# Optimization experiments

Measured on AMD Instinct MI355X. Metric: run time of the kernel, lower is better.

## Reference

```python
import jax, jax.numpy as jnp
import numpy as np

IN_F, OUT_F = 4096, 11008
IN_G, OUT_G = 8, 1
NUM_CB, CB_SIZE = 2, 256


def setup_inputs() -> dict:
    key = jax.random.key(0)
    k1, k2, k3, k4, k5 = jax.random.split(key, 5)
    no, ni = OUT_F // OUT_G, IN_F // IN_G
    x = jax.random.normal(k1, (4, 2048, IN_F), dtype=jnp.float32)
    codes = jax.random.randint(k2, (no, ni, NUM_CB), 0, CB_SIZE, dtype=jnp.int32)
    codebooks = jax.random.normal(k3, (NUM_CB, CB_SIZE, OUT_G, IN_G), dtype=jnp.float32)
    scales = jax.random.uniform(k4, (no, 1, 1, 1), dtype=jnp.float32) + 0.5
    bias = jax.random.normal(k5, (OUT_F,), dtype=jnp.float32)
    return {"x": x, "codes": codes, "codebooks": codebooks, "scales": scales, "bias": bias}


def _dequantize_weight(codes, codebooks, scales):
    # codes: [no, ni, M] ints; codebooks: [M, C, og, ig]; scales: [no, 1, 1, 1]
    M = codebooks.shape[0]
    og, ig = codebooks.shape[2], codebooks.shape[3]
    no, ni = codes.shape[0], codes.shape[1]
    # gather each codebook's entry and sum over codebooks -> [no, ni, og, ig]
    m_idx = jnp.arange(M)[None, None, :]
    gathered = codebooks[m_idx, codes]            # [no, ni, M, og, ig]
    deq = gathered.sum(axis=2) * scales           # [no, ni, og, ig]
    # reorder groups back to dense weight [out_features, in_features]
    return deq.transpose(0, 2, 1, 3).reshape(no * og, ni * ig)


def reference(x, codes, codebooks, scales, bias):
    w = _dequantize_weight(codes, codebooks, scales)  # [OUT_F, IN_F]
    return jnp.einsum("bsi,oi->bso", x, w) + bias
```

## Files before the change

### kernel.cpp

```cpp
#include <hip/hip_runtime.h>
#include <hip/hip_bf16.h>
#include <stdint.h>

#define IN_F   4096
#define OUT_F  11008
#define M_TOK  8192

typedef __attribute__((ext_vector_type(4))) int   int32x4;

__device__ __forceinline__ float block_rowmax(float m, float* red, int t) {
    red[t] = m; __syncthreads();
    for (int s = 128; s > 0; s >>= 1) {
        if (t < s) red[t] = fmaxf(red[t], red[t + s]);
        __syncthreads();
    }
    float r = red[0]; __syncthreads();
    return fmaxf(r, 1e-8f);
}

__global__ __launch_bounds__(256) void k_qx(
        const float* __restrict__ x, signed char* __restrict__ Xq,
        float* __restrict__ sx) {
    __shared__ float red[256];
    int r = blockIdx.x, t = threadIdx.x;
    const float4* xr = (const float4*)(x + (size_t)r * IN_F) + t * 4;
    float4 v0 = xr[0], v1 = xr[1], v2 = xr[2], v3 = xr[3];
    float m = 0.f;
#define MX4(v) m = fmaxf(m, fmaxf(fmaxf(fabsf(v.x), fabsf(v.y)), fmaxf(fabsf(v.z), fabsf(v.w))))
    MX4(v0); MX4(v1); MX4(v2); MX4(v3);
    float rm = block_rowmax(m, red, t);
    if (t == 0) sx[r] = rm / 127.f;
    float inv = 127.f / rm;
    union { signed char c[16]; uint4 u; } pk;
#define Q4(v, o) pk.c[o] = (signed char)__float2int_rn(v.x * inv);            \
                 pk.c[o+1] = (signed char)__float2int_rn(v.y * inv);          \
                 pk.c[o+2] = (signed char)__float2int_rn(v.z * inv);          \
                 pk.c[o+3] = (signed char)__float2int_rn(v.w * inv)
    Q4(v0, 0); Q4(v1, 4); Q4(v2, 8); Q4(v3, 12);
    *(uint4*)(Xq + (size_t)r * IN_F + t * 16) = pk.u;
}

__global__ __launch_bounds__(256) void k_qw(
        const int* __restrict__ codes,
        const float* __restrict__ codebooks,
        const float* __restrict__ scales,
        signed char* __restrict__ Wq, float* __restrict__ sw) {
    __shared__ float cb[4096];
    __shared__ float red[256];
    int o = blockIdx.x, t = threadIdx.x;
    {
        const float4* cbg = (const float4*)codebooks;
        float4* cbl = (float4*)cb;
#pragma unroll
        for (int i = 0; i < 4; ++i) cbl[t + i * 256] = cbg[t + i * 256];
    }
    __syncthreads();
    const int2* cp = (const int2*)codes + (size_t)o * 512 + t * 2;
    int2 c0 = cp[0], c1 = cp[1];
    float e[16]; float m = 0.f;
#pragma unroll
    for (int j = 0; j < 8; ++j) {
        e[j]     = cb[c0.x * 8 + j] + cb[2048 + c0.y * 8 + j];
        e[8 + j] = cb[c1.x * 8 + j] + cb[2048 + c1.y * 8 + j];
    }
#pragma unroll
    for (int j = 0; j < 16; ++j) m = fmaxf(m, fabsf(e[j]));
    float rm = block_rowmax(m, red, t);
    if (t == 0) sw[o] = scales[o] * rm / 127.f;
    float inv = 127.f / rm;
    union { signed char c[16]; uint4 u; } pk;
#pragma unroll
    for (int j = 0; j < 16; ++j) pk.c[j] = (signed char)__float2int_rn(e[j] * inv);
    *(uint4*)(Wq + (size_t)o * IN_F + t * 16) = pk.u;
}


#define BARRIER() __builtin_amdgcn_s_barrier()
#define VMW(n)    asm volatile("s_waitcnt vmcnt(" #n ")")

#define GL16(gp, lp) __builtin_amdgcn_global_load_lds(                        \
    (const __attribute__((address_space(1))) void*)(gp),                      \
    (__attribute__((address_space(3))) void*)(lp), 16, 0, 0)

__global__ __launch_bounds__(512, 2) void k_gemm(
        const signed char* __restrict__ A,
        const signed char* __restrict__ B,
        const float* __restrict__ sx,
        const float* __restrict__ sw,
        const float* __restrict__ bias,
        float* __restrict__ out) {
    __shared__ signed char lA0[256 * 128];
    __shared__ signed char lA1[256 * 128];
    __shared__ signed char lB0[256 * 128];
    __shared__ signed char lB1[256 * 128];

    const int tid = threadIdx.x;
    const int l = tid & 63;
    const int w = tid >> 6;
    const int wm = w >> 2, wn = w & 3;

    int lid = blockIdx.x;
    int xcd = lid & 7, j = lid >> 3;
    int bx = j >> 2;
    int by = (xcd << 2) + (j & 3);
    const int rowBase = by * 256;
    const int colBase = bx * 256;

    const int srow = w * 8 + (l >> 3);
    const int scol = ((l & 7) ^ ((l >> 3) & 7)) << 4;
    const signed char* gA = A + (size_t)(rowBase + srow) * IN_F + scol;
    const signed char* gB = B + (size_t)(colBase + srow) * IN_F + scol;
    signed char* lA0w = &lA0[w * 8 * 128];
    signed char* lA1w = &lA1[w * 8 * 128];
    signed char* lB0w = &lB0[w * 8 * 128];
    signed char* lB1w = &lB1[w * 8 * 128];

#define STAGEQ_(P, t, q) do {                                                 \
    const signed char* _g = (((q) < 2) ? gA : gB) + (size_t)(t) * 128;        \
    signed char* _l = (((q) < 2) ? lA##P##w : lB##P##w);                      \
    const int _r = ((q) & 1) * 128;                                           \
    GL16(_g + (size_t)_r * IN_F,        _l + _r * 128);                       \
    GL16(_g + (size_t)(_r + 64) * IN_F, _l + (_r + 64) * 128);                \
} while (0)

    const int frow = l & 15, g = l >> 4;
    const int cho0 = ((g ^ (frow & 7)) << 4);
    const int cho1 = (((4 + g) ^ (frow & 7)) << 4);
    const char* rowA0 = (const char*)&lA0[(wm * 128 + frow) * 128];
    const char* rowA1 = (const char*)&lA1[(wm * 128 + frow) * 128];
    const char* rowB0 = (const char*)&lB0[(wn * 64 + frow) * 128];
    const char* rowB1 = (const char*)&lB1[(wn * 64 + frow) * 128];
#define LDA_(P, m, kk) (*(const int32x4*)(rowA##P + (m) * 2048 + ((kk) ? cho1 : cho0)))
#define LDB_(P, n, kk) (*(const int32x4*)(rowB##P + (n) * 2048 + ((kk) ? cho1 : cho0)))

    int32x4 acc[8][4] = {};
    int32x4 ar[4][2], br[4][2];

#define QUAD(M0, N0) do {                                                     \
    __builtin_amdgcn_s_setprio(1);                                            \
    _Pragma("unroll") for (int mm = 0; mm < 4; ++mm)                          \
    _Pragma("unroll") for (int nn = 0; nn < 2; ++nn)                          \
    _Pragma("unroll") for (int kk = 0; kk < 2; ++kk)                          \
        acc[(M0) + mm][(N0) + nn] = __builtin_amdgcn_mfma_i32_16x16x64_i8(    \
            ar[mm][kk], br[(N0) + nn][kk], acc[(M0) + mm][(N0) + nn], 0, 0, 0);\
    __builtin_amdgcn_s_setprio(0);                                            \
} while (0)

#define RD_A03_B01(P) do {                                                    \
    _Pragma("unroll") for (int mm = 0; mm < 4; ++mm) {                        \
        ar[mm][0] = LDA_(P, mm, 0); ar[mm][1] = LDA_(P, mm, 1); }             \
    br[0][0] = LDB_(P, 0, 0); br[0][1] = LDB_(P, 0, 1);                       \
    br[1][0] = LDB_(P, 1, 0); br[1][1] = LDB_(P, 1, 1);                       \
} while (0)
#define RD_B23(P) do {                                                        \
    br[2][0] = LDB_(P, 2, 0); br[2][1] = LDB_(P, 2, 1);                       \
    br[3][0] = LDB_(P, 3, 0); br[3][1] = LDB_(P, 3, 1);                       \
} while (0)
#define RD_A47(P) do {                                                        \
    _Pragma("unroll") for (int mm = 0; mm < 4; ++mm) {                        \
        ar[mm][0] = LDA_(P, 4 + mm, 0); ar[mm][1] = LDA_(P, 4 + mm, 1); }     \
} while (0)

    STAGEQ_(0, 0, 0); STAGEQ_(0, 0, 1); STAGEQ_(0, 0, 2); STAGEQ_(0, 0, 3);
    STAGEQ_(1, 1, 2); STAGEQ_(1, 1, 3);
    VMW(4); BARRIER();

    for (int i = 0; i < 15; ++i) {
        int e = 2 * i, o = 2 * i + 1;
        RD_A03_B01(0);
        STAGEQ_(1, o, 0); STAGEQ_(1, o, 1);
        QUAD(0, 0);
        RD_B23(0);
        QUAD(0, 2);
        BARRIER();
        RD_A47(0);
        STAGEQ_(0, e + 2, 2); STAGEQ_(0, e + 2, 3);
        QUAD(4, 2); QUAD(4, 0);
        VMW(4); BARRIER();
        RD_A03_B01(1);
        STAGEQ_(0, e + 2, 0); STAGEQ_(0, e + 2, 1);
        QUAD(0, 0);
        RD_B23(1);
        QUAD(0, 2);
        BARRIER();
        RD_A47(1);
        STAGEQ_(1, o + 2, 2); STAGEQ_(1, o + 2, 3);
        QUAD(4, 2); QUAD(4, 0);
        VMW(4); BARRIER();
    }

    RD_A03_B01(0);
    STAGEQ_(1, 31, 0); STAGEQ_(1, 31, 1);
    QUAD(0, 0);
    RD_B23(0);
    QUAD(0, 2);
    BARRIER();
    RD_A47(0);
    QUAD(4, 2); QUAD(4, 0);
    VMW(0); BARRIER();
    RD_A03_B01(1);
    QUAD(0, 0);
    RD_B23(1);
    QUAD(0, 2);
    RD_A47(1);
    QUAD(4, 2); QUAD(4, 0);

#pragma unroll
    for (int n = 0; n < 4; ++n) {
        int gcol = colBase + wn * 64 + n * 16 + frow;
        float swv = sw[gcol];
        float bv = bias[gcol];
#pragma unroll
        for (int m = 0; m < 8; ++m) {
            int grow0 = rowBase + wm * 128 + m * 16 + g * 4;
            float4 sx4 = *(const float4*)&sx[grow0];
            out[(size_t)(grow0 + 0) * OUT_F + gcol] = (float)acc[m][n][0] * sx4.x * swv + bv;
            out[(size_t)(grow0 + 1) * OUT_F + gcol] = (float)acc[m][n][1] * sx4.y * swv + bv;
            out[(size_t)(grow0 + 2) * OUT_F + gcol] = (float)acc[m][n][2] * sx4.z * swv + bv;
            out[(size_t)(grow0 + 3) * OUT_F + gcol] = (float)acc[m][n][3] * sx4.w * swv + bv;
        }
    }
}

extern "C" void kernel_launch(void* const* d_in, const int* in_sizes, int n_in,
                              void* d_out, int out_size, void* d_ws, size_t ws_size,
                              hipStream_t stream) {
    const float* x         = (const float*)d_in[0];
    const int*   codes     = (const int*)d_in[1];
    const float* codebooks = (const float*)d_in[2];
    const float* scales    = (const float*)d_in[3];
    const float* bias      = (const float*)d_in[4];
    float* out = (float*)d_out;

    signed char* Wq = (signed char*)d_ws;
    signed char* Xq = Wq + (size_t)OUT_F * IN_F;
    float* sx = (float*)(Xq + (size_t)M_TOK * IN_F);
    float* sw = sx + M_TOK;

    k_qx<<<M_TOK, 256, 0, stream>>>(x, Xq, sx);
    k_qw<<<OUT_F, 256, 0, stream>>>(codes, codebooks, scales, Wq, sw);
    k_gemm<<<1376, 512, 0, stream>>>(Xq, Wq, sx, sw, bias, out);
}
```

Baseline: 470.8 us.

## Restructure int8 GEMM main loop into HipKittens-style 8-wave ping-pong schedule

Reorganizes the K-loop so that LDS-to-register reads of the next tile overlap with MFMA quadrants of the current one, using split B register buffers (brA/brB) so B fragments can be prefetched while the others are in use. Global-to-LDS staging is regrouped into per-matrix halves and placed between compute phases, with extra barriers per stage. The aim is to hide LDS read latency behind MFMA issue. In exchange it adds barriers and more live registers, and the hazard ordering between staging writes and reads has to be reasoned about carefully.

```diff
diff --git a/kernel.cpp b/kernel.cpp
--- a/kernel.cpp
+++ b/kernel.cpp
@@ -115,12 +115,13 @@
     signed char* lB0w = &lB0[w * 8 * 128];
     signed char* lB1w = &lB1[w * 8 * 128];
 
-#define STAGEQ_(P, t, q) do {                                                 \
-    const signed char* _g = (((q) < 2) ? gA : gB) + (size_t)(t) * 128;        \
-    signed char* _l = (((q) < 2) ? lA##P##w : lB##P##w);                      \
-    const int _r = ((q) & 1) * 128;                                           \
-    GL16(_g + (size_t)_r * IN_F,        _l + _r * 128);                       \
-    GL16(_g + (size_t)(_r + 64) * IN_F, _l + (_r + 64) * 128);                \
+#define STAGEH_(P, t, H) do {                                                 \
+    const signed char* _g = ((H) ? gB : gA) + (size_t)(t) * 128;              \
+    signed char* _l = ((H) ? lB##P##w : lA##P##w);                            \
+    GL16(_g,                       _l);                                       \
+    GL16(_g +  64 * IN_F,          _l +  64 * 128);                           \
+    GL16(_g + 128 * IN_F,          _l + 128 * 128);                           \
+    GL16(_g + 192 * IN_F,          _l + 192 * 128);                           \
 } while (0)
 
     const int frow = l & 15, g = l >> 4;
@@ -134,76 +135,93 @@
 #define LDB_(P, n, kk) (*(const int32x4*)(rowB##P + (n) * 2048 + ((kk) ? cho1 : cho0)))
 
     int32x4 acc[8][4] = {};
-    int32x4 ar[4][2], br[4][2];
-
-#define QUAD(M0, N0) do {                                                     \
+    int32x4 ar[4][2];
+    int32x4 brA[2][2];
+    int32x4 brB[2][2];
+
+#define QUADQ(M0, N0, BR) do {                                                \
     __builtin_amdgcn_s_setprio(1);                                            \
     _Pragma("unroll") for (int mm = 0; mm < 4; ++mm)                          \
     _Pragma("unroll") for (int nn = 0; nn < 2; ++nn)                          \
     _Pragma("unroll") for (int kk = 0; kk < 2; ++kk)                          \
         acc[(M0) + mm][(N0) + nn] = __builtin_amdgcn_mfma_i32_16x16x64_i8(    \
-            ar[mm][kk], br[(N0) + nn][kk], acc[(M0) + mm][(N0) + nn], 0, 0, 0);\
+            ar[mm][kk], BR[nn][kk], acc[(M0) + mm][(N0) + nn], 0, 0, 0);      \
     __builtin_amdgcn_s_setprio(0);                                            \
 } while (0)
 
-#define RD_A03_B01(P) do {                                                    \
+#define RD_AR03(P) do {                                                       \
     _Pragma("unroll") for (int mm = 0; mm < 4; ++mm) {                        \
         ar[mm][0] = LDA_(P, mm, 0); ar[mm][1] = LDA_(P, mm, 1); }             \
-    br[0][0] = LDB_(P, 0, 0); br[0][1] = LDB_(P, 0, 1);                       \
-    br[1][0] = LDB_(P, 1, 0); br[1][1] = LDB_(P, 1, 1);                       \
-} while (0)
-#define RD_B23(P) do {                                                        \
-    br[2][0] = LDB_(P, 2, 0); br[2][1] = LDB_(P, 2, 1);                       \
-    br[3][0] = LDB_(P, 3, 0); br[3][1] = LDB_(P, 3, 1);                       \
-} while (0)
-#define RD_A47(P) do {                                                        \
+} while (0)
+#define RD_AR47(P) do {                                                       \
     _Pragma("unroll") for (int mm = 0; mm < 4; ++mm) {                        \
         ar[mm][0] = LDA_(P, 4 + mm, 0); ar[mm][1] = LDA_(P, 4 + mm, 1); }     \
 } while (0)
-
-    STAGEQ_(0, 0, 0); STAGEQ_(0, 0, 1); STAGEQ_(0, 0, 2); STAGEQ_(0, 0, 3);
-    STAGEQ_(1, 1, 2); STAGEQ_(1, 1, 3);
+#define RD_BR01(P) do {                                                       \
+    brA[0][0] = LDB_(P, 0, 0); brA[0][1] = LDB_(P, 0, 1);                     \
+    brA[1][0] = LDB_(P, 1, 0); brA[1][1] = LDB_(P, 1, 1);                     \
+} while (0)
+#define RD_BR23(P) do {                                                       \
+    brB[0][0] = LDB_(P, 2, 0); brB[0][1] = LDB_(P, 2, 1);                     \
+    brB[1][0] = LDB_(P, 3, 0); brB[1][1] = LDB_(P, 3, 1);                     \
+} while (0)
+
+    STAGEH_(0, 0, 0); STAGEH_(0, 0, 1);
+    STAGEH_(1, 1, 1);
     VMW(4); BARRIER();
+    RD_AR03(0); RD_BR01(0);
+    STAGEH_(1, 1, 0);
+    BARRIER();
 
     for (int i = 0; i < 15; ++i) {
-        int e = 2 * i, o = 2 * i + 1;
-        RD_A03_B01(0);
-        STAGEQ_(1, o, 0); STAGEQ_(1, o, 1);
-        QUAD(0, 0);
-        RD_B23(0);
-        QUAD(0, 2);
-        BARRIER();
-        RD_A47(0);
-        STAGEQ_(0, e + 2, 2); STAGEQ_(0, e + 2, 3);
-        QUAD(4, 2); QUAD(4, 0);
+        int t = 2 * i;
+        QUADQ(0, 0, brA);
+        RD_BR23(0);
+        BARRIER();
+        QUADQ(0, 2, brB);
+        RD_AR47(0);
+        BARRIER();
+        QUADQ(4, 2, brB);
+        STAGEH_(0, t + 2, 1);
         VMW(4); BARRIER();
-        RD_A03_B01(1);
-        STAGEQ_(0, e + 2, 0); STAGEQ_(0, e + 2, 1);
-        QUAD(0, 0);
-        RD_B23(1);
-        QUAD(0, 2);
-        BARRIER();
-        RD_A47(1);
-        STAGEQ_(1, o + 2, 2); STAGEQ_(1, o + 2, 3);
-        QUAD(4, 2); QUAD(4, 0);
+        QUADQ(4, 0, brA);
+        RD_AR03(1); RD_BR01(1);
+        STAGEH_(0, t + 2, 0);
+        BARRIER();
+        QUADQ(0, 0, brA);
+        RD_BR23(1);
+        BARRIER();
+        QUADQ(0, 2, brB);
+        RD_AR47(1);
+        BARRIER();
+        QUADQ(4, 2, brB);
+        STAGEH_(1, t + 3, 1);
         VMW(4); BARRIER();
-    }
-
-    RD_A03_B01(0);
-    STAGEQ_(1, 31, 0); STAGEQ_(1, 31, 1);
-    QUAD(0, 0);
-    RD_B23(0);
-    QUAD(0, 2);
-    BARRIER();
-    RD_A47(0);
-    QUAD(4, 2); QUAD(4, 0);
+        QUADQ(4, 0, brA);
+        RD_AR03(0); RD_BR01(0);
+        STAGEH_(1, t + 3, 0);
+        BARRIER();
+    }
+
+    QUADQ(0, 0, brA);
+    RD_BR23(0);
+    BARRIER();
+    QUADQ(0, 2, brB);
+    RD_AR47(0);
+    BARRIER();
+    QUADQ(4, 2, brB);
     VMW(0); BARRIER();
-    RD_A03_B01(1);
-    QUAD(0, 0);
-    RD_B23(1);
-    QUAD(0, 2);
-    RD_A47(1);
-    QUAD(4, 2); QUAD(4, 0);
+    QUADQ(4, 0, brA);
+    RD_AR03(1); RD_BR01(1);
+    BARRIER();
+    QUADQ(0, 0, brA);
+    RD_BR23(1);
+    BARRIER();
+    QUADQ(0, 2, brB);
+    RD_AR47(1);
+    BARRIER();
+    QUADQ(4, 2, brB);
+    QUADQ(4, 0, brA);
 
 #pragma unroll
     for (int n = 0; n < 4; ++n) {
```

Measured after the change: 469.6 us. Within noise of the previous version (-0.3%).
